# Kernel tuning notes

Measured on AMD Instinct MI355X. Metric: run time of the kernel, lower is better.

## Reference

```python
import jax, jax.numpy as jnp
import numpy as np

N = 50000        # nodes
E = 800000       # edges (avg degree 16)
H = 128          # hidden_nf
IN_NODE = 11     # in_node_nf
IN_EDGE = 4      # in_edge_nf
L = 4            # n_layers


def _lin_init(key, fan_in, fan_out, layers=None):
    shape = (fan_in, fan_out) if layers is None else (layers, fan_in, fan_out)
    return jax.random.normal(key, shape, dtype=jnp.float32) / np.sqrt(fan_in)


def setup_inputs() -> dict:
    key = jax.random.key(0)
    ks = jax.random.split(key, 16)
    edge_in = 2 * H + 1 + IN_EDGE   # [h_row, h_col, radial, edge_attr]
    node_in = H + H + IN_NODE       # [h, agg, h0]
    return {
        "h0": jax.random.normal(ks[0], (N, IN_NODE), dtype=jnp.float32),
        "x": jax.random.normal(ks[1], (N, 3), dtype=jnp.float32),
        "edge_index": jax.random.randint(ks[2], (2, E), 0, N),
        "edge_attr": jax.random.normal(ks[3], (E, IN_EDGE), dtype=jnp.float32),
        "node_mask": jnp.ones((N, 1), dtype=jnp.float32),
        "edge_mask": jnp.ones((E, 1), dtype=jnp.float32),
        "n_nodes": N,
        "emb_w": _lin_init(ks[4], IN_NODE, H),
        "emb_b": jnp.zeros((H,), dtype=jnp.float32),
        "ew1": _lin_init(ks[5], edge_in, H, L),
        "eb1": jnp.zeros((L, H), dtype=jnp.float32),
        "ew2": _lin_init(ks[6], H, H, L),
        "eb2": jnp.zeros((L, H), dtype=jnp.float32),
        "nw1": _lin_init(ks[7], node_in, H, L),
        "nb1": jnp.zeros((L, H), dtype=jnp.float32),
        "nw2": _lin_init(ks[8], H, H, L),
        "nb2": jnp.zeros((L, H), dtype=jnp.float32),
    }


def reference(h0, x, edge_index, edge_attr, node_mask, edge_mask, n_nodes,
              emb_w, emb_b, ew1, eb1, ew2, eb2, nw1, nb1, nw2, nb2):
    row, col = edge_index[0], edge_index[1]
    num_nodes = h0.shape[0]
    # coord2radial (coords never updated since coord_model is not called)
    coord_diff = x[row] - x[col]                               # [E, 3]
    radial = jnp.sum(coord_diff * coord_diff, axis=1, keepdims=True)  # [E, 1]

    h = h0 @ emb_w + emb_b                                     # embedding, [N, H]
    for i in range(L):
        # edge model
        edge_in = jnp.concatenate([h[row], h[col], radial, edge_attr], axis=1)
        m = jax.nn.silu(edge_in @ ew1[i] + eb1[i])
        m = jax.nn.silu(m @ ew2[i] + eb2[i])
        m = m * edge_mask                                      # [E, H]
        # node model: scatter-sum messages, concat with h and node_attr=h0
        agg = jax.ops.segment_sum(m, row, num_segments=num_nodes)  # [N, H]
        node_in = jnp.concatenate([h, agg, h0], axis=1)
        out = jax.nn.silu(node_in @ nw1[i] + nb1[i]) @ nw2[i] + nb2[i]
        h = h + out                                            # recurrent residual
    return h
```

## Files before the change

### kernel.cpp

```cpp
#include <hip/hip_runtime.h>

#define NN 50000
#define NE 800000
#define HD 128
#define INN 11
#define NL 4
#define NG16 3125
#define BTS 132
#define K1S 292

typedef __attribute__((ext_vector_type(8))) short bf16x8;
typedef __attribute__((ext_vector_type(4))) float f32x4;

__device__ __forceinline__ float silu_f(float x) {
    return x * __builtin_amdgcn_rcpf(1.0f + __expf(-x));
}

__device__ __forceinline__ short f2bf(float x) {
    unsigned u = __float_as_uint(x);
    return (short)((u + 0x7FFFu + ((u >> 16) & 1u)) >> 16);
}
__device__ __forceinline__ unsigned f2bf2u(float lo, float hi) {
    unsigned a = __float_as_uint(lo), b = __float_as_uint(hi);
    a = (a + 0x7FFFu + ((a >> 16) & 1u)) >> 16;
    b = (b + 0x7FFFu + ((b >> 16) & 1u)) & 0xFFFF0000u;
    return a | b;
}
__device__ __forceinline__ bf16x8 pack8(float4 a, float4 b) {
    bf16x8 r;
    r[0] = f2bf(a.x); r[1] = f2bf(a.y); r[2] = f2bf(a.z); r[3] = f2bf(a.w);
    r[4] = f2bf(b.x); r[5] = f2bf(b.y); r[6] = f2bf(b.z); r[7] = f2bf(b.w);
    return r;
}

__global__ __launch_bounds__(256) void embed_kernel(
    const float* __restrict__ h0, const float* __restrict__ w,
    const float* __restrict__ b, float* __restrict__ h)
{
    int idx = blockIdx.x * 256 + threadIdx.x;
    if (idx >= NN * HD) return;
    int n = idx >> 7, j = idx & 127;
    float acc = b[j];
    #pragma unroll
    for (int k = 0; k < INN; ++k)
        acc += h0[n * INN + k] * w[k * HD + j];
    h[idx] = acc;
}

__global__ __launch_bounds__(256) void csr_zero(int* __restrict__ cnt)
{
    int i = blockIdx.x * 256 + threadIdx.x;
    if (i < NN) cnt[i] = 0;
}

__global__ __launch_bounds__(256) void csr_hist(const int* __restrict__ ei, int* __restrict__ cnt)
{
    int e = blockIdx.x * 256 + threadIdx.x;
    atomicAdd(&cnt[ei[e]], 1);
}

__global__ __launch_bounds__(1024) void csr_scan(
    const int* __restrict__ cnt, int* __restrict__ rowptr, int* __restrict__ cursor)
{
    __shared__ int part[1024];
    int t = threadIdx.x;
    int base = t * 49;
    int s = 0;
    for (int i = 0; i < 49; ++i) { int j = base + i; if (j < NN) s += cnt[j]; }
    part[t] = s;
    __syncthreads();
    for (int off = 1; off < 1024; off <<= 1) {
        int v = (t >= off) ? part[t - off] : 0;
        __syncthreads();
        part[t] += v;
        __syncthreads();
    }
    int run = (t == 0) ? 0 : part[t - 1];
    for (int i = 0; i < 49; ++i) {
        int j = base + i;
        if (j < NN) { rowptr[j] = run; cursor[j] = run; run += cnt[j]; }
    }
    if (t == 1023) rowptr[NN] = part[1023];
}

__global__ __launch_bounds__(256) void csr_fill(
    const int* __restrict__ ei, int* __restrict__ cursor, int* __restrict__ eidx)
{
    int e = blockIdx.x * 256 + threadIdx.x;
    int r = ei[e];
    int p = atomicAdd(&cursor[r], 1);
    eidx[p] = e;
}

__global__ __launch_bounds__(256) void edge_pre(
    const int* __restrict__ ei, const int* __restrict__ eidx,
    const float* __restrict__ x, const float* __restrict__ eattr,
    const float* __restrict__ emask,
    int4* __restrict__ ed_p, float4* __restrict__ ea_p)
{
    int p = blockIdx.x * 256 + threadIdx.x;
    int e = eidx[p];
    int r = ei[e], c = ei[NE + e];
    float dx = x[3 * r]     - x[3 * c];
    float dy = x[3 * r + 1] - x[3 * c + 1];
    float dz = x[3 * r + 2] - x[3 * c + 2];
    float rad = dx * dx + dy * dy + dz * dz;
    ed_p[p] = make_int4(r * 64, c * 64, __float_as_int(rad), __float_as_int(emask[e]));
    ea_p[p] = ((const float4*)eattr)[e];
}

__global__ __launch_bounds__(512) void tu_mfma(
    const float* __restrict__ h, const float* __restrict__ ew1_l,
    short* __restrict__ tb, short* __restrict__ ub)
{
    __shared__ __align__(16) short BT[128 * BTS];
    const float* wsrc = ew1_l + (blockIdx.y ? 128 * HD : 0);
    short* outp = blockIdx.y ? ub : tb;
    for (int i = threadIdx.x; i < 128 * 128; i += 512) {
        int c = i >> 7, k = i & 127;
        BT[c * BTS + k] = f2bf(wsrc[k * HD + c]);
    }
    int wv = threadIdx.x >> 6, lane = threadIdx.x & 63;
    int ln15 = lane & 15, quad = lane >> 4;
    __syncthreads();

    for (int g = blockIdx.x * 8 + wv; g < NG16; g += gridDim.x * 8) {
        int row = g * 16 + ln15;
        const float* hrow = h + row * HD;
        bf16x8 afr[4];
        #pragma unroll
        for (int kt = 0; kt < 4; ++kt) {
            float4 x0 = *(const float4*)(hrow + kt * 32 + quad * 8);
            float4 x1 = *(const float4*)(hrow + kt * 32 + quad * 8 + 4);
            afr[kt] = pack8(x0, x1);
        }
        #pragma unroll
        for (int ct = 0; ct < 8; ++ct) {
            f32x4 acc = {0.f, 0.f, 0.f, 0.f};
            #pragma unroll
            for (int kt = 0; kt < 4; ++kt) {
                bf16x8 bfr = *(const bf16x8*)&BT[(ct * 16 + ln15) * BTS + kt * 32 + quad * 8];
                acc = __builtin_amdgcn_mfma_f32_16x16x32_bf16(afr[kt], bfr, acc, 0, 0, 0);
            }
            int col = ct * 16 + ln15;
            #pragma unroll
            for (int r4 = 0; r4 < 4; ++r4) {
                int orow = g * 16 + quad * 4 + r4;
                outp[orow * HD + col] = f2bf(acc[r4]);
            }
        }
    }
}

__global__ __launch_bounds__(512, 4) void edge_m_kernel(
    const short* __restrict__ tb, const short* __restrict__ ub,
    const int4* __restrict__ ed_p, const float4* __restrict__ ea_p,
    const int* __restrict__ rowptr,
    const float* __restrict__ ew1_l, const float* __restrict__ eb1_l,
    const float* __restrict__ ew2_l, const float* __restrict__ eb2_l,
    float* __restrict__ agg)
{
    __shared__ __align__(16) short BT[128 * BTS];
    __shared__ __align__(16) short VA[8][16 * BTS];
    __shared__ float s_b2[128];

    for (int i = threadIdx.x; i < 128 * 128; i += 512) {
        int k = i >> 7, n = i & 127;
        BT[n * BTS + k] = f2bf(ew2_l[i]);
    }
    if (threadIdx.x < 128) s_b2[threadIdx.x] = eb2_l[threadIdx.x];

    int cp = threadIdx.x & 63;
    int c0 = cp * 2;
    float wr0  = ew1_l[256 * HD + c0],     wr1  = ew1_l[256 * HD + c0 + 1];
    float wa00 = ew1_l[257 * HD + c0],     wa01 = ew1_l[257 * HD + c0 + 1];
    float wa10 = ew1_l[258 * HD + c0],     wa11 = ew1_l[258 * HD + c0 + 1];
    float wa20 = ew1_l[259 * HD + c0],     wa21 = ew1_l[259 * HD + c0 + 1];
    float wa30 = ew1_l[260 * HD + c0],     wa31 = ew1_l[260 * HD + c0 + 1];
    float b10  = eb1_l[c0],                b11  = eb1_l[c0 + 1];

    int lane = threadIdx.x & 63;
    int wv   = threadIdx.x >> 6;
    int ln15 = lane & 15;
    int quad = lane >> 4;
    short* VAw = &VA[wv][0];
    const unsigned* tb32 = (const unsigned*)tb;
    const unsigned* ub32 = (const unsigned*)ub;
    __syncthreads();

    for (int n = blockIdx.x * 8 + wv; n < NN; n += gridDim.x * 8) {
        int s = rowptr[n], en = rowptr[n + 1];
        unsigned tw = tb32[n * 64 + cp];
        float t0 = __uint_as_float(tw << 16);
        float t1 = __uint_as_float(tw & 0xFFFF0000u);

        float sums[8];
        #pragma unroll
        for (int ct = 0; ct < 8; ++ct) sums[ct] = 0.f;

        unsigned uwv[16];
        float    radv[16];

        #pragma unroll
        for (int i = 0; i < 16; ++i) {
            int p = s + i;
            int4 ed = (p < en) ? ed_p[p] : make_int4(0, 0, 0, 0);
            radv[i] = __int_as_float(ed.z);
            uwv[i]  = ub32[ed.y + cp];
        }

        for (int base = s; base < en; base += 16) {
            int pr = base + quad * 4;
            float mk0 = (pr + 0 < en) ? __int_as_float(ed_p[pr + 0].w) : 0.f;
            float mk1 = (pr + 1 < en) ? __int_as_float(ed_p[pr + 1].w) : 0.f;
            float mk2 = (pr + 2 < en) ? __int_as_float(ed_p[pr + 2].w) : 0.f;
            float mk3 = (pr + 3 < en) ? __int_as_float(ed_p[pr + 3].w) : 0.f;

            #pragma unroll
            for (int i = 0; i < 16; ++i) {
                int p = base + i;
                unsigned out = 0u;
                if (p < en) {
                    float4 ea = ea_p[p];
                    float u0 = __uint_as_float(uwv[i] << 16);
                    float u1 = __uint_as_float(uwv[i] & 0xFFFF0000u);
                    float base0 = radv[i] * wr0 + ea.x * wa00 + ea.y * wa10 + ea.z * wa20 + ea.w * wa30 + b10;
                    float base1 = radv[i] * wr1 + ea.x * wa01 + ea.y * wa11 + ea.z * wa21 + ea.w * wa31 + b11;
                    out = f2bf2u(silu_f(t0 + u0 + base0), silu_f(t1 + u1 + base1));
                }
                *(unsigned*)&VAw[i * BTS + c0] = out;
            }

            __builtin_amdgcn_wave_barrier();
            __builtin_amdgcn_s_waitcnt(0xc07f);

            bf16x8 afr[4];
            #pragma unroll
            for (int kt = 0; kt < 4; ++kt)
                afr[kt] = *(const bf16x8*)&VAw[ln15 * BTS + kt * 32 + quad * 8];

            __builtin_amdgcn_wave_barrier();

            int nb = base + 16;
            if (nb < en) {
                #pragma unroll
                for (int i = 0; i < 16; ++i) {
                    int p = nb + i;
                    int4 ed = (p < en) ? ed_p[p] : make_int4(0, 0, 0, 0);
                    radv[i] = __int_as_float(ed.z);
                    uwv[i]  = ub32[ed.y + cp];
                }
            }

            #pragma unroll
            for (int ct = 0; ct < 8; ++ct) {
                f32x4 acc = {0.f, 0.f, 0.f, 0.f};
                #pragma unroll
                for (int kt = 0; kt < 4; ++kt) {
                    bf16x8 bfr = *(const bf16x8*)&BT[(ct * 16 + ln15) * BTS + kt * 32 + quad * 8];
                    acc = __builtin_amdgcn_mfma_f32_16x16x32_bf16(afr[kt], bfr, acc, 0, 0, 0);
                }
                float b2c = s_b2[ct * 16 + ln15];
                sums[ct] += silu_f(acc[0] + b2c) * mk0 + silu_f(acc[1] + b2c) * mk1
                          + silu_f(acc[2] + b2c) * mk2 + silu_f(acc[3] + b2c) * mk3;
            }
        }

        #pragma unroll
        for (int ct = 0; ct < 8; ++ct) {
            float v = sums[ct];
            v += __shfl_xor(v, 16, 64);
            v += __shfl_xor(v, 32, 64);
            sums[ct] = v;
        }
        float vA = (quad & 2) ? ((quad & 1) ? sums[6] : sums[4])
                              : ((quad & 1) ? sums[2] : sums[0]);
        float vB = (quad & 2) ? ((quad & 1) ? sums[7] : sums[5])
                              : ((quad & 1) ? sums[3] : sums[1]);
        int colA = quad * 32 + ln15;
        agg[n * HD + colA]      = vA;
        agg[n * HD + colA + 16] = vB;
    }
}

__global__ __launch_bounds__(512) void nk1_mfma(
    const float* __restrict__ h, const float* __restrict__ agg,
    const float* __restrict__ h0,
    const float* __restrict__ nw1_l, const float* __restrict__ nb1_l,
    short* __restrict__ qb)
{
    __shared__ __align__(16) short BT[64 * K1S];
    int c0 = blockIdx.y * 64;
    for (int i = threadIdx.x; i < 64 * 288; i += 512) {
        int c = i / 288, k = i - c * 288;
        BT[c * K1S + k] = (k < 267) ? f2bf(nw1_l[k * HD + c0 + c]) : (short)0;
    }
    int wv = threadIdx.x >> 6, lane = threadIdx.x & 63;
    int ln15 = lane & 15, quad = lane >> 4;
    __syncthreads();

    for (int g = blockIdx.x * 8 + wv; g < NG16; g += gridDim.x * 8) {
        int row = g * 16 + ln15;
        const float* hrow = h + row * HD;
        const float* arow = agg + row * HD;
        bf16x8 afr[9];
        #pragma unroll
        for (int kt = 0; kt < 4; ++kt) {
            float4 x0 = *(const float4*)(hrow + kt * 32 + quad * 8);
            float4 x1 = *(const float4*)(hrow + kt * 32 + quad * 8 + 4);
            afr[kt] = pack8(x0, x1);
        }
        #pragma unroll
        for (int kt = 0; kt < 4; ++kt) {
            float4 x0 = *(const float4*)(arow + kt * 32 + quad * 8);
            float4 x1 = *(const float4*)(arow + kt * 32 + quad * 8 + 4);
            afr[4 + kt] = pack8(x0, x1);
        }
        {
            bf16x8 a8 = {0, 0, 0, 0, 0, 0, 0, 0};
            if (quad == 0) {
                #pragma unroll
                for (int jj = 0; jj < 8; ++jj) a8[jj] = f2bf(h0[row * INN + jj]);
            } else if (quad == 1) {
                #pragma unroll
                for (int jj = 0; jj < 3; ++jj) a8[jj] = f2bf(h0[row * INN + 8 + jj]);
            }
            afr[8] = a8;
        }
        #pragma unroll
        for (int ct = 0; ct < 4; ++ct) {
            f32x4 acc = {0.f, 0.f, 0.f, 0.f};
            #pragma unroll
            for (int kt = 0; kt < 9; ++kt) {
                bf16x8 bfr = *(const bf16x8*)&BT[(ct * 16 + ln15) * K1S + kt * 32 + quad * 8];
                acc = __builtin_amdgcn_mfma_f32_16x16x32_bf16(afr[kt], bfr, acc, 0, 0, 0);
            }
            int col = c0 + ct * 16 + ln15;
            float b = nb1_l[col];
            #pragma unroll
            for (int r4 = 0; r4 < 4; ++r4) {
                int orow = g * 16 + quad * 4 + r4;
                qb[orow * HD + col] = f2bf(silu_f(acc[r4] + b));
            }
        }
    }
}

__global__ __launch_bounds__(512) void nk2_mfma(
    const short* __restrict__ qb, const float* __restrict__ nw2_l,
    const float* __restrict__ nb2_l, float* __restrict__ h)
{
    __shared__ __align__(16) short BT[128 * BTS];
    for (int i = threadIdx.x; i < 128 * 128; i += 512) {
        int c = i >> 7, k = i & 127;
        BT[c * BTS + k] = f2bf(nw2_l[k * HD + c]);
    }
    int wv = threadIdx.x >> 6, lane = threadIdx.x & 63;
    int ln15 = lane & 15, quad = lane >> 4;
    __syncthreads();

    for (int g = blockIdx.x * 8 + wv; g < NG16; g += gridDim.x * 8) {
        int row = g * 16 + ln15;
        bf16x8 afr[4];
        #pragma unroll
        for (int kt = 0; kt < 4; ++kt)
            afr[kt] = *(const bf16x8*)(qb + row * HD + kt * 32 + quad * 8);

        #pragma unroll
        for (int ct = 0; ct < 8; ++ct) {
            f32x4 acc = {0.f, 0.f, 0.f, 0.f};
            #pragma unroll
            for (int kt = 0; kt < 4; ++kt) {
                bf16x8 bfr = *(const bf16x8*)&BT[(ct * 16 + ln15) * BTS + kt * 32 + quad * 8];
                acc = __builtin_amdgcn_mfma_f32_16x16x32_bf16(afr[kt], bfr, acc, 0, 0, 0);
            }
            int col = ct * 16 + ln15;
            float b = nb2_l[col];
            #pragma unroll
            for (int r4 = 0; r4 < 4; ++r4) {
                int orow = g * 16 + quad * 4 + r4;
                h[orow * HD + col] += acc[r4] + b;
            }
        }
    }
}

extern "C" void kernel_launch(void* const* d_in, const int* in_sizes, int n_in,
                              void* d_out, int out_size, void* d_ws, size_t ws_size,
                              hipStream_t stream)
{
    const float* h0    = (const float*)d_in[0];
    const float* x     = (const float*)d_in[1];
    const int*   ei    = (const int*)d_in[2];
    const float* eattr = (const float*)d_in[3];
    const float* emask = (const float*)d_in[5];
    const float* emb_w = (const float*)d_in[7];
    const float* emb_b = (const float*)d_in[8];
    const float* ew1   = (const float*)d_in[9];
    const float* eb1   = (const float*)d_in[10];
    const float* ew2   = (const float*)d_in[11];
    const float* eb2   = (const float*)d_in[12];
    const float* nw1   = (const float*)d_in[13];
    const float* nb1   = (const float*)d_in[14];
    const float* nw2   = (const float*)d_in[15];
    const float* nb2   = (const float*)d_in[16];

    float* h = (float*)d_out;

    short*  tb     = (short*)d_ws;
    short*  ub     = tb + (size_t)NN * HD;
    float*  agg    = (float*)(ub + (size_t)NN * HD);
    short*  qb     = tb;
    int*    cnt    = (int*)(agg + (size_t)NN * HD);
    int*    rowptr = cnt + NN;
    int*    cursor = rowptr + NN + 1;
    int*    eidx   = cursor + NN;
    int4*   ed_p   = (int4*)(eidx + NE + 1);
    float4* ea_p   = (float4*)(ed_p + NE);

    csr_zero<<<(NN + 255) / 256, 256, 0, stream>>>(cnt);
    csr_hist<<<NE / 256, 256, 0, stream>>>(ei, cnt);
    csr_scan<<<1, 1024, 0, stream>>>(cnt, rowptr, cursor);
    csr_fill<<<NE / 256, 256, 0, stream>>>(ei, cursor, eidx);
    edge_pre<<<NE / 256, 256, 0, stream>>>(ei, eidx, x, eattr, emask, ed_p, ea_p);

    embed_kernel<<<(NN * HD + 255) / 256, 256, 0, stream>>>(h0, emb_w, emb_b, h);

    dim3 gtu(128, 2);
    dim3 gn1(128, 2);
    for (int l = 0; l < NL; ++l) {
        tu_mfma<<<gtu, 512, 0, stream>>>(h, ew1 + l * 261 * HD, tb, ub);
        edge_m_kernel<<<512, 512, 0, stream>>>(tb, ub, ed_p, ea_p, rowptr,
            ew1 + l * 261 * HD, eb1 + l * HD, ew2 + l * HD * HD, eb2 + l * HD, agg);
        nk1_mfma<<<gn1, 512, 0, stream>>>(h, agg, h0,
            nw1 + l * 267 * HD, nb1 + l * HD, qb);
        nk2_mfma<<<128, 512, 0, stream>>>(qb, nw2 + l * HD * HD, nb2 + l * HD, h);
    }
}
```

Baseline: 1.589 ms.

## Split fused edge kernel into first-layer materialization and MFMA aggregation passes

The fused per-node edge kernel is split into two kernels. The first computes the first edge-MLP layer (silu of t+u+radial/attr terms) for every edge in sorted order and writes it to a bf16 buffer, gathering edge_attr through eidx. The second reads 16-edge tiles of that buffer directly as MFMA operands, applies the second layer and the segment sum, and writes agg as bf16, which nk1 now loads without conversion. This removes the per-wave LDS staging and the serial gather-then-compute dependency, but adds a write and read of about 200 MB of intermediate edge activations per layer and an extra kernel launch, and agg is now stored at lower precision.

```diff
diff --git a/kernel.cpp b/kernel.cpp
--- a/kernel.cpp
+++ b/kernel.cpp
@@ -94,9 +94,8 @@
 
 __global__ __launch_bounds__(256) void edge_pre(
     const int* __restrict__ ei, const int* __restrict__ eidx,
-    const float* __restrict__ x, const float* __restrict__ eattr,
-    const float* __restrict__ emask,
-    int4* __restrict__ ed_p, float4* __restrict__ ea_p)
+    const float* __restrict__ x, const float* __restrict__ emask,
+    int4* __restrict__ ed_p)
 {
     int p = blockIdx.x * 256 + threadIdx.x;
     int e = eidx[p];
@@ -106,7 +105,11 @@
     float dz = x[3 * r + 2] - x[3 * c + 2];
     float rad = dx * dx + dy * dy + dz * dz;
     ed_p[p] = make_int4(r * 64, c * 64, __float_as_int(rad), __float_as_int(emask[e]));
-    ea_p[p] = ((const float4*)eattr)[e];
+}
+
+__global__ __launch_bounds__(1024) void vpad_zero(unsigned* __restrict__ vb32)
+{
+    vb32[(size_t)NE * 64 + threadIdx.x] = 0u;
 }
 
 __global__ __launch_bounds__(512) void tu_mfma(
@@ -152,24 +155,13 @@
     }
 }
 
-__global__ __launch_bounds__(512, 4) void edge_m_kernel(
+__global__ __launch_bounds__(512) void edge_v_kernel(
     const short* __restrict__ tb, const short* __restrict__ ub,
-    const int4* __restrict__ ed_p, const float4* __restrict__ ea_p,
-    const int* __restrict__ rowptr,
+    const int4* __restrict__ ed_p, const int* __restrict__ eidx,
+    const float* __restrict__ eattr,
     const float* __restrict__ ew1_l, const float* __restrict__ eb1_l,
-    const float* __restrict__ ew2_l, const float* __restrict__ eb2_l,
-    float* __restrict__ agg)
-{
-    __shared__ __align__(16) short BT[128 * BTS];
-    __shared__ __align__(16) short VA[8][16 * BTS];
-    __shared__ float s_b2[128];
-
-    for (int i = threadIdx.x; i < 128 * 128; i += 512) {
-        int k = i >> 7, n = i & 127;
-        BT[n * BTS + k] = f2bf(ew2_l[i]);
-    }
-    if (threadIdx.x < 128) s_b2[threadIdx.x] = eb2_l[threadIdx.x];
-
+    short* __restrict__ vbuf)
+{
     int cp = threadIdx.x & 63;
     int c0 = cp * 2;
     float wr0  = ew1_l[256 * HD + c0],     wr1  = ew1_l[256 * HD + c0 + 1];
@@ -179,78 +171,80 @@
     float wa30 = ew1_l[260 * HD + c0],     wa31 = ew1_l[260 * HD + c0 + 1];
     float b10  = eb1_l[c0],                b11  = eb1_l[c0 + 1];
 
+    const unsigned* tb32 = (const unsigned*)tb;
+    const unsigned* ub32 = (const unsigned*)ub;
+    const float4*   ea4  = (const float4*)eattr;
+    unsigned*       vb32 = (unsigned*)vbuf;
+
+    int w  = (blockIdx.x * 512 + threadIdx.x) >> 6;
+    int nw = gridDim.x * 8;
+
+    for (int p0 = w * 4; p0 < NE; p0 += nw * 4) {
+        int4 edv[4]; unsigned twv[4], uwv[4]; float4 eav[4];
+        #pragma unroll
+        for (int j = 0; j < 4; ++j) edv[j] = ed_p[p0 + j];
+        #pragma unroll
+        for (int j = 0; j < 4; ++j) {
+            twv[j] = tb32[edv[j].x + cp];
+            uwv[j] = ub32[edv[j].y + cp];
+            eav[j] = ea4[eidx[p0 + j]];
+        }
+        #pragma unroll
+        for (int j = 0; j < 4; ++j) {
+            float rad = __int_as_float(edv[j].z);
+            float t0 = __uint_as_float(twv[j] << 16);
+            float t1 = __uint_as_float(twv[j] & 0xFFFF0000u);
+            float u0 = __uint_as_float(uwv[j] << 16);
+            float u1 = __uint_as_float(uwv[j] & 0xFFFF0000u);
+            float s0 = t0 + u0 + rad * wr0 + eav[j].x * wa00 + eav[j].y * wa10
+                     + eav[j].z * wa20 + eav[j].w * wa30 + b10;
+            float s1 = t1 + u1 + rad * wr1 + eav[j].x * wa01 + eav[j].y * wa11
+                     + eav[j].z * wa21 + eav[j].w * wa31 + b11;
+            vb32[(size_t)(p0 + j) * 64 + cp] = f2bf2u(silu_f(s0), silu_f(s1));
+        }
+    }
+}
+
+__global__ __launch_bounds__(512) void edge_agg_kernel(
+    const short* __restrict__ vbuf, const int4* __restrict__ ed_p,
+    const int* __restrict__ rowptr,
+    const float* __restrict__ ew2_l, const float* __restrict__ eb2_l,
+    short* __restrict__ aggb)
+{
+    __shared__ __align__(16) short BT[128 * BTS];
+    __shared__ float s_b2[128];
+
+    for (int i = threadIdx.x; i < 128 * 128; i += 512) {
+        int k = i >> 7, n = i & 127;
+        BT[n * BTS + k] = f2bf(ew2_l[i]);
+    }
+    if (threadIdx.x < 128) s_b2[threadIdx.x] = eb2_l[threadIdx.x];
+
     int lane = threadIdx.x & 63;
     int wv   = threadIdx.x >> 6;
     int ln15 = lane & 15;
     int quad = lane >> 4;
-    short* VAw = &VA[wv][0];
-    const unsigned* tb32 = (const unsigned*)tb;
-    const unsigned* ub32 = (const unsigned*)ub;
     __syncthreads();
 
     for (int n = blockIdx.x * 8 + wv; n < NN; n += gridDim.x * 8) {
         int s = rowptr[n], en = rowptr[n + 1];
-        unsigned tw = tb32[n * 64 + cp];
-        float t0 = __uint_as_float(tw << 16);
-        float t1 = __uint_as_float(tw & 0xFFFF0000u);
 
         float sums[8];
         #pragma unroll
         for (int ct = 0; ct < 8; ++ct) sums[ct] = 0.f;
 
-        unsigned uwv[16];
-        float    radv[16];
-
-        #pragma unroll
-        for (int i = 0; i < 16; ++i) {
-            int p = s + i;
-            int4 ed = (p < en) ? ed_p[p] : make_int4(0, 0, 0, 0);
-            radv[i] = __int_as_float(ed.z);
-            uwv[i]  = ub32[ed.y + cp];
-        }
-
         for (int base = s; base < en; base += 16) {
+            const short* vrow = vbuf + (size_t)(base + ln15) * HD + quad * 8;
+            bf16x8 afr[4];
+            #pragma unroll
+            for (int kt = 0; kt < 4; ++kt)
+                afr[kt] = *(const bf16x8*)(vrow + kt * 32);
+
             int pr = base + quad * 4;
             float mk0 = (pr + 0 < en) ? __int_as_float(ed_p[pr + 0].w) : 0.f;
             float mk1 = (pr + 1 < en) ? __int_as_float(ed_p[pr + 1].w) : 0.f;
             float mk2 = (pr + 2 < en) ? __int_as_float(ed_p[pr + 2].w) : 0.f;
             float mk3 = (pr + 3 < en) ? __int_as_float(ed_p[pr + 3].w) : 0.f;
-
-            #pragma unroll
-            for (int i = 0; i < 16; ++i) {
-                int p = base + i;
-                unsigned out = 0u;
-                if (p < en) {
-                    float4 ea = ea_p[p];
-                    float u0 = __uint_as_float(uwv[i] << 16);
-                    float u1 = __uint_as_float(uwv[i] & 0xFFFF0000u);
-                    float base0 = radv[i] * wr0 + ea.x * wa00 + ea.y * wa10 + ea.z * wa20 + ea.w * wa30 + b10;
-                    float base1 = radv[i] * wr1 + ea.x * wa01 + ea.y * wa11 + ea.z * wa21 + ea.w * wa31 + b11;
-                    out = f2bf2u(silu_f(t0 + u0 + base0), silu_f(t1 + u1 + base1));
-                }
-                *(unsigned*)&VAw[i * BTS + c0] = out;
-            }
-
-            __builtin_amdgcn_wave_barrier();
-            __builtin_amdgcn_s_waitcnt(0xc07f);
-
-            bf16x8 afr[4];
-            #pragma unroll
-            for (int kt = 0; kt < 4; ++kt)
-                afr[kt] = *(const bf16x8*)&VAw[ln15 * BTS + kt * 32 + quad * 8];
-
-            __builtin_amdgcn_wave_barrier();
-
-            int nb = base + 16;
-            if (nb < en) {
-                #pragma unroll
-                for (int i = 0; i < 16; ++i) {
-                    int p = nb + i;
-                    int4 ed = (p < en) ? ed_p[p] : make_int4(0, 0, 0, 0);
-                    radv[i] = __int_as_float(ed.z);
-                    uwv[i]  = ub32[ed.y + cp];
-                }
-            }
 
             #pragma unroll
             for (int ct = 0; ct < 8; ++ct) {
@@ -278,13 +272,13 @@
         float vB = (quad & 2) ? ((quad & 1) ? sums[7] : sums[5])
                               : ((quad & 1) ? sums[3] : sums[1]);
         int colA = quad * 32 + ln15;
-        agg[n * HD + colA]      = vA;
-        agg[n * HD + colA + 16] = vB;
+        aggb[(size_t)n * HD + colA]      = f2bf(vA);
+        aggb[(size_t)n * HD + colA + 16] = f2bf(vB);
     }
 }
 
 __global__ __launch_bounds__(512) void nk1_mfma(
-    const float* __restrict__ h, const float* __restrict__ agg,
+    const float* __restrict__ h, const short* __restrict__ aggb,
     const float* __restrict__ h0,
     const float* __restrict__ nw1_l, const float* __restrict__ nb1_l,
     short* __restrict__ qb)
@@ -302,7 +296,6 @@
     for (int g = blockIdx.x * 8 + wv; g < NG16; g += gridDim.x * 8) {
         int row = g * 16 + ln15;
         const float* hrow = h + row * HD;
-        const float* arow = agg + row * HD;
         bf16x8 afr[9];
         #pragma unroll
         for (int kt = 0; kt < 4; ++kt) {
@@ -311,11 +304,8 @@
             afr[kt] = pack8(x0, x1);
         }
         #pragma unroll
-        for (int kt = 0; kt < 4; ++kt) {
-            float4 x0 = *(const float4*)(arow + kt * 32 + quad * 8);
-            float4 x1 = *(const float4*)(arow + kt * 32 + quad * 8 + 4);
-            afr[4 + kt] = pack8(x0, x1);
-        }
+        for (int kt = 0; kt < 4; ++kt)
+            afr[4 + kt] = *(const bf16x8*)(aggb + (size_t)row * HD + kt * 32 + quad * 8);
         {
             bf16x8 a8 = {0, 0, 0, 0, 0, 0, 0, 0};
             if (quad == 0) {
@@ -409,20 +399,21 @@
 
     short*  tb     = (short*)d_ws;
     short*  ub     = tb + (size_t)NN * HD;
-    float*  agg    = (float*)(ub + (size_t)NN * HD);
+    short*  aggb   = ub + (size_t)NN * HD;
+    short*  vbuf   = aggb + (size_t)NN * HD;
+    int4*   ed_p   = (int4*)(vbuf + (size_t)(NE + 16) * HD);
+    int*    rowptr = (int*)(ed_p + NE);
+    int*    cnt    = rowptr + NN + 1;
+    int*    cursor = cnt + NN;
+    int*    eidx   = cursor + NN;
     short*  qb     = tb;
-    int*    cnt    = (int*)(agg + (size_t)NN * HD);
-    int*    rowptr = cnt + NN;
-    int*    cursor = rowptr + NN + 1;
-    int*    eidx   = cursor + NN;
-    int4*   ed_p   = (int4*)(eidx + NE + 1);
-    float4* ea_p   = (float4*)(ed_p + NE);
 
     csr_zero<<<(NN + 255) / 256, 256, 0, stream>>>(cnt);
     csr_hist<<<NE / 256, 256, 0, stream>>>(ei, cnt);
     csr_scan<<<1, 1024, 0, stream>>>(cnt, rowptr, cursor);
     csr_fill<<<NE / 256, 256, 0, stream>>>(ei, cursor, eidx);
-    edge_pre<<<NE / 256, 256, 0, stream>>>(ei, eidx, x, eattr, emask, ed_p, ea_p);
+    edge_pre<<<NE / 256, 256, 0, stream>>>(ei, eidx, x, emask, ed_p);
+    vpad_zero<<<1, 1024, 0, stream>>>((unsigned*)vbuf);
 
     embed_kernel<<<(NN * HD + 255) / 256, 256, 0, stream>>>(h0, emb_w, emb_b, h);
 
@@ -430,9 +421,11 @@
     dim3 gn1(128, 2);
     for (int l = 0; l < NL; ++l) {
         tu_mfma<<<gtu, 512, 0, stream>>>(h, ew1 + l * 261 * HD, tb, ub);
-        edge_m_kernel<<<512, 512, 0, stream>>>(tb, ub, ed_p, ea_p, rowptr,
-            ew1 + l * 261 * HD, eb1 + l * HD, ew2 + l * HD * HD, eb2 + l * HD, agg);
-        nk1_mfma<<<gn1, 512, 0, stream>>>(h, agg, h0,
+        edge_v_kernel<<<1024, 512, 0, stream>>>(tb, ub, ed_p, eidx, eattr,
+            ew1 + l * 261 * HD, eb1 + l * HD, vbuf);
+        edge_agg_kernel<<<1024, 512, 0, stream>>>(vbuf, ed_p, rowptr,
+            ew2 + l * HD * HD, eb2 + l * HD, aggb);
+        nk1_mfma<<<gn1, 512, 0, stream>>>(h, aggb, h0,
             nw1 + l * 267 * HD, nb1 + l * HD, qb);
         nk2_mfma<<<128, 512, 0, stream>>>(qb, nw2 + l * HD * HD, nb2 + l * HD, h);
     }
```

New measurement: 1.559 ms. Within noise of the previous version (-1.9%).
